# Optimization experiments

Hardware: AMD Instinct MI355X
Metric: run time of the kernel (lower is better)

The kernel has to match this reference:

```python
import jax, jax.numpy as jnp
import numpy as np

N = 30000
E = 480000
F_IN = 16
HID = 64
HEADS = 2
D = HID // HEADS
L = 2
NEG_SLOPE = 0.2


def _edge_softmax(alpha, dst, num_nodes):
    # alpha: [E, HEADS]; softmax over edges sharing the same destination node
    amax = jax.ops.segment_max(alpha, dst, num_segments=num_nodes)
    ex = jnp.exp(alpha - amax[dst])
    den = jax.ops.segment_sum(ex, dst, num_segments=num_nodes)
    return ex / (den[dst] + 1e-16)


def _han_edge(x_src, x_dst, ei, a_src, a_dst, n_dst):
    # x_src: [N_src, HEADS, D], x_dst: [N_dst, HEADS, D], ei: [2, E]
    src, dst = ei[0], ei[1]
    a_s = jnp.einsum('nhd,hd->nh', x_src, a_src)
    a_d = jnp.einsum('nhd,hd->nh', x_dst, a_dst)
    alpha = jax.nn.leaky_relu(a_s[src] + a_d[dst], NEG_SLOPE)  # [E, HEADS]
    alpha = _edge_softmax(alpha, dst, n_dst)
    msg = x_src[src] * alpha[..., None]                        # [E, HEADS, D]
    out = jax.ops.segment_sum(msg, dst, num_segments=n_dst)
    return jax.nn.relu(out.reshape(n_dst, HID))


def _group(xs, q, kw, kb):
    # semantic (cross-relation) attention; xs: list of [N, HID]
    out = jnp.stack(xs)                           # [T, N, HID]
    k = jnp.tanh(out @ kw + kb).mean(axis=1)      # [T, HID]
    attn = jax.nn.softmax(jnp.einsum('f,tf->t', q, k))
    return jnp.einsum('t,tnf->nf', attn, out)


def setup_inputs() -> dict:
    key = jax.random.key(0)
    ks = jax.random.split(key, 24)
    s = 0.1
    f32 = jnp.float32
    return {
        'x_job': jax.random.normal(ks[0], (N, F_IN), f32),
        'x_machine': jax.random.normal(ks[1], (N, F_IN), f32),
        'edge_index_jm': jax.random.randint(ks[2], (2, E), 0, N),
        'edge_index_mj': jax.random.randint(ks[3], (2, E), 0, N),
        'edge_index_jj': jax.random.randint(ks[4], (2, E), 0, N),
        'enc_w_job': jax.random.normal(ks[5], (F_IN, HID), f32) * s,
        'enc_b_job': jax.random.normal(ks[6], (HID,), f32) * s,
        'enc_w_machine': jax.random.normal(ks[7], (F_IN, HID), f32) * s,
        'enc_b_machine': jax.random.normal(ks[8], (HID,), f32) * s,
        'proj_w': jax.random.normal(ks[9], (L, 2, HID, HID), f32) * s,
        'proj_b': jax.random.normal(ks[10], (L, 2, HID), f32) * s,
        'att_src': jax.random.normal(ks[11], (L, 3, HEADS, D), f32) * s,
        'att_dst': jax.random.normal(ks[12], (L, 3, HEADS, D), f32) * s,
        'klin_w': jax.random.normal(ks[13], (L, HID, HID), f32) * s,
        'klin_b': jax.random.normal(ks[14], (L, HID), f32) * s,
        'q_sem': jax.random.normal(ks[15], (L, HID), f32) * s,
        'lin0_w': jax.random.normal(ks[16], (HID, HID), f32) * s,
        'lin0_b': jax.random.normal(ks[17], (HID,), f32) * s,
        'linout_w': jax.random.normal(ks[18], (HID, 16), f32) * s,
        'linout_b': jax.random.normal(ks[19], (16,), f32) * s,
        'linv_w': jax.random.normal(ks[20], (HID, 1), f32) * s,
        'linv_b': jax.random.normal(ks[21], (1,), f32) * s,
    }


def reference(x_job, x_machine, edge_index_jm, edge_index_mj, edge_index_jj,
              enc_w_job, enc_b_job, enc_w_machine, enc_b_machine,
              proj_w, proj_b, att_src, att_dst, klin_w, klin_b, q_sem,
              lin0_w, lin0_b, linout_w, linout_b, linv_w, linv_b):
    # per-node-type encoder: Linear + relu_
    xj = jax.nn.relu(x_job @ enc_w_job + enc_b_job)          # [N, HID]
    xm = jax.nn.relu(x_machine @ enc_w_machine + enc_b_machine)
    for l in range(L):
        pj = (xj @ proj_w[l, 0] + proj_b[l, 0]).reshape(N, HEADS, D)
        pm = (xm @ proj_w[l, 1] + proj_b[l, 1]).reshape(N, HEADS, D)
        # edge-type order follows edge_index_dict iteration: jm, mj, jj
        out_jm = _han_edge(pj, pm, edge_index_jm, att_src[l, 0], att_dst[l, 0], N)
        out_mj = _han_edge(pm, pj, edge_index_mj, att_src[l, 1], att_dst[l, 1], N)
        out_jj = _han_edge(pj, pj, edge_index_jj, att_src[l, 2], att_dst[l, 2], N)
        xj = _group([out_mj, out_jj], q_sem[l], klin_w[l], klin_b[l])
        xm = _group([out_jm], q_sem[l], klin_w[l], klin_b[l])
    full_x = jnp.concatenate([xj, xm], axis=0)               # [2N, HID]
    value = (full_x @ linv_w + linv_b).mean()
    h = full_x @ lin0_w + lin0_b
    action = jnp.tanh(h @ linout_w + linout_b)               # [2N, 16]
    return action, value
```

## Files before the change

### kernel.cpp

```cpp
#include <hip/hip_runtime.h>
#include <math.h>


#define GEMM_GRID 512
#define KRED_GRID 256
#define BUCKET_SHIFT 6
#define BUCKET_NODES 64
#define BUCKET_CAP 1536
#define BIN_CHUNK 2048

__device__ __forceinline__ float4 ld4(const float* __restrict__ p, int idx4)
{
    return ((const float4*)p)[idx4];
}

__device__ __forceinline__ float halfred(float v)
{
#pragma unroll
    for (int off = 16; off; off >>= 1) v += __shfl_xor(v, off);
    return v;
}

struct ProjSide {
    const float* x0; const float* x1; const float* attn;
    const float* W; const float* b; float* p;
    const float* a0v; float* o0; const float* a1v; float* o1;
    const float* a2v; float* o2; const float* a3v; float* o3;
};

__global__ __launch_bounds__(256, 4) void proj2_kernel(ProjSide sa, ProjSide sb, int n)
{
    const ProjSide S = blockIdx.y ? sb : sa;
    __shared__ __align__(16) float xs[16][64];
    int tid = threadIdx.x, lane = tid & 63, wid = tid >> 6;
    float Wreg[64];
#pragma unroll
    for (int k = 0; k < 64; k++) Wreg[k] = S.W[k * 64 + lane];
    float bc = S.b[lane];
    float a0c = S.o0 ? S.a0v[lane] : 0.f;
    float a1c = S.o1 ? S.a1v[lane] : 0.f;
    float a2c = S.o2 ? S.a2v[lane] : 0.f;
    float a3c = S.o3 ? S.a3v[lane] : 0.f;
    float ca0 = 0.f, ca1 = 0.f;
    if (S.x1) { ca0 = S.attn[0]; ca1 = S.attn[1]; }
    int qn = tid >> 4, qq = tid & 15;
    for (int base = blockIdx.x * 16; base < n; base += gridDim.x * 16) {
        __syncthreads();
        int node = base + qn;
        if (node < n) {
            float4 xq;
            if (S.x1) {
                float4 u = ld4(S.x0, node * 16 + qq), v = ld4(S.x1, node * 16 + qq);
                xq.x = ca0 * u.x + ca1 * v.x; xq.y = ca0 * u.y + ca1 * v.y;
                xq.z = ca0 * u.z + ca1 * v.z; xq.w = ca0 * u.w + ca1 * v.w;
            } else {
                xq = ld4(S.x0, node * 16 + qq);
            }
            *(float4*)&xs[qn][qq * 4] = xq;
        }
        __syncthreads();
#pragma unroll
        for (int nd = 0; nd < 4; nd++) {
            int nc = base + wid * 4 + nd;
            if (nc >= n) break;
            float acc = bc;
#pragma unroll
            for (int k4 = 0; k4 < 16; k4++) {
                float4 xv = *(const float4*)&xs[wid * 4 + nd][k4 * 4];
                acc = fmaf(xv.x, Wreg[4 * k4 + 0], acc);
                acc = fmaf(xv.y, Wreg[4 * k4 + 1], acc);
                acc = fmaf(xv.z, Wreg[4 * k4 + 2], acc);
                acc = fmaf(xv.w, Wreg[4 * k4 + 3], acc);
            }
            S.p[nc * 64 + lane] = acc;
            int h = lane >> 5;
            if (S.o0) { float v = halfred(acc * a0c); if ((lane & 31) == 0) S.o0[nc * 2 + h] = v; }
            if (S.o1) { float v = halfred(acc * a1c); if ((lane & 31) == 0) S.o1[nc * 2 + h] = v; }
            if (S.o2) { float v = halfred(acc * a2c); if ((lane & 31) == 0) S.o2[nc * 2 + h] = v; }
            if (S.o3) { float v = halfred(acc * a3c); if ((lane & 31) == 0) S.o3[nc * 2 + h] = v; }
        }
    }
}

struct EncSide {
    const float* x; const float* We; const float* be;
    const float* W; const float* b; float* p;
    const float* a0v; float* o0; const float* a1v; float* o1;
    const float* a2v; float* o2; const float* a3v; float* o3;
};

__global__ __launch_bounds__(256, 4) void encproj2_kernel(EncSide sa, EncSide sb, int n)
{
    const EncSide S = blockIdx.y ? sb : sa;
    __shared__ __align__(16) float xs[16][16];
    __shared__ __align__(16) float es[16][64];
    int tid = threadIdx.x, lane = tid & 63, wid = tid >> 6;
    float Ereg[16];
#pragma unroll
    for (int k = 0; k < 16; k++) Ereg[k] = S.We[k * 64 + lane];
    float Wreg[64];
#pragma unroll
    for (int k = 0; k < 64; k++) Wreg[k] = S.W[k * 64 + lane];
    float ebc = S.be[lane], bc = S.b[lane];
    float a0c = S.o0 ? S.a0v[lane] : 0.f;
    float a1c = S.o1 ? S.a1v[lane] : 0.f;
    float a2c = S.o2 ? S.a2v[lane] : 0.f;
    float a3c = S.o3 ? S.a3v[lane] : 0.f;
    for (int base = blockIdx.x * 16; base < n; base += gridDim.x * 16) {
        __syncthreads();
        if (tid < 64) {
            int nn = tid >> 2, q = tid & 3;
            int node = base + nn;
            if (node < n) *(float4*)&xs[nn][q * 4] = ld4(S.x, node * 4 + q);
        }
        __syncthreads();
#pragma unroll
        for (int nd = 0; nd < 4; nd++) {
            int nc = base + wid * 4 + nd;
            if (nc >= n) break;
            float a = ebc;
#pragma unroll
            for (int k4 = 0; k4 < 4; k4++) {
                float4 xv = *(const float4*)&xs[wid * 4 + nd][k4 * 4];
                a = fmaf(xv.x, Ereg[4 * k4 + 0], a);
                a = fmaf(xv.y, Ereg[4 * k4 + 1], a);
                a = fmaf(xv.z, Ereg[4 * k4 + 2], a);
                a = fmaf(xv.w, Ereg[4 * k4 + 3], a);
            }
            es[wid * 4 + nd][lane] = fmaxf(a, 0.f);
        }
        __syncthreads();
#pragma unroll
        for (int nd = 0; nd < 4; nd++) {
            int nc = base + wid * 4 + nd;
            if (nc >= n) break;
            float acc = bc;
#pragma unroll
            for (int k4 = 0; k4 < 16; k4++) {
                float4 xv = *(const float4*)&es[wid * 4 + nd][k4 * 4];
                acc = fmaf(xv.x, Wreg[4 * k4 + 0], acc);
                acc = fmaf(xv.y, Wreg[4 * k4 + 1], acc);
                acc = fmaf(xv.z, Wreg[4 * k4 + 2], acc);
                acc = fmaf(xv.w, Wreg[4 * k4 + 3], acc);
            }
            S.p[nc * 64 + lane] = acc;
            int h = lane >> 5;
            if (S.o0) { float v = halfred(acc * a0c); if ((lane & 31) == 0) S.o0[nc * 2 + h] = v; }
            if (S.o1) { float v = halfred(acc * a1c); if ((lane & 31) == 0) S.o1[nc * 2 + h] = v; }
            if (S.o2) { float v = halfred(acc * a2c); if ((lane & 31) == 0) S.o2[nc * 2 + h] = v; }
            if (S.o3) { float v = halfred(acc * a3c); if ((lane & 31) == 0) S.o3[nc * 2 + h] = v; }
        }
    }
}

__global__ __launch_bounds__(256) void bin_kernel(
    const int* __restrict__ s0, const int* __restrict__ s1, const int* __restrict__ s2,
    const int* __restrict__ d0, const int* __restrict__ d1, const int* __restrict__ d2,
    int* __restrict__ cursor, int* __restrict__ binned, int e, int nb)
{
    int ty = blockIdx.y;
    const int* s = ty == 0 ? s0 : (ty == 1 ? s1 : s2);
    const int* d = ty == 0 ? d0 : (ty == 1 ? d1 : d2);
    __shared__ int cnt[512], rbase[512];
    int tid = threadIdx.x;
    for (int i = tid; i < nb; i += 256) cnt[i] = 0;
    __syncthreads();
    int beg = blockIdx.x * BIN_CHUNK;
    int end = beg + BIN_CHUNK; if (end > e) end = e;
    for (int i = beg + tid; i < end; i += 256)
        atomicAdd(&cnt[d[i] >> BUCKET_SHIFT], 1);
    __syncthreads();
    for (int i = tid; i < nb; i += 256) {
        rbase[i] = atomicAdd(&cursor[ty * nb + i], cnt[i]);
        cnt[i] = 0;
    }
    __syncthreads();
    int* bb = binned + (size_t)ty * nb * BUCKET_CAP;
    for (int i = beg + tid; i < end; i += 256) {
        int dv = d[i], b = dv >> BUCKET_SHIFT;
        int slot = rbase[b] + atomicAdd(&cnt[b], 1);
        if (slot < BUCKET_CAP)
            bb[b * BUCKET_CAP + slot] = (s[i] << BUCKET_SHIFT) | (dv & (BUCKET_NODES - 1));
    }
}

__global__ void bucketscan_kernel(const int* __restrict__ cursor,
                                  int* __restrict__ bbase, int nb)
{
    int ty = blockIdx.x;
    const int* c = cursor + (size_t)ty * nb;
    int* o = bbase + (size_t)ty * nb;
    int lane = threadIdx.x;
    int carry = 0;
    for (int base = 0; base < nb; base += 64) {
        int i = base + lane;
        int v = (i < nb) ? c[i] : 0;
        int incl = v;
#pragma unroll
        for (int off = 1; off < 64; off <<= 1) {
            int u = __shfl_up(incl, off);
            if (lane >= off) incl += u;
        }
        if (i < nb) o[i] = carry + incl - v;
        carry += __shfl(incl, 63);
    }
}

__global__ __launch_bounds__(256) void bucket_kernel(
    const int* __restrict__ cursor, const int* __restrict__ bbase,
    const int* __restrict__ binned,
    int* __restrict__ rowptr, int* __restrict__ rowend, int* __restrict__ colsrc,
    int n, int nb, int e)
{
    int ty = blockIdx.y, b = blockIdx.x;
    __shared__ int stage[BUCKET_CAP];
    __shared__ int ncnt[64], nexcl[64], ncur[64];
    int tid = threadIdx.x;
    int cnt = cursor[ty * nb + b]; if (cnt > BUCKET_CAP) cnt = BUCKET_CAP;
    int base = bbase[ty * nb + b];
    const int* bb = binned + ((size_t)ty * nb + b) * BUCKET_CAP;
    if (tid < 64) ncnt[tid] = 0;
    __syncthreads();
    for (int i = tid; i < cnt; i += 256) {
        int v = bb[i];
        stage[i] = v;
        atomicAdd(&ncnt[v & (BUCKET_NODES - 1)], 1);
    }
    __syncthreads();
    if (tid < 64) {
        int v = ncnt[tid];
        int incl = v;
#pragma unroll
        for (int off = 1; off < 64; off <<= 1) {
            int u = __shfl_up(incl, off);
            if (tid >= off) incl += u;
        }
        int excl = incl - v;
        nexcl[tid] = excl;
        ncur[tid] = 0;
        int node = (b << BUCKET_SHIFT) + tid;
        if (node < n) {
            rowptr[(size_t)ty * n + node] = base + excl;
            rowend[(size_t)ty * n + node] = base + excl + v;
        }
    }
    __syncthreads();
    int* cs = colsrc + (size_t)ty * e;
    for (int i = tid; i < cnt; i += 256) {
        int v = stage[i];
        int dl = v & (BUCKET_NODES - 1);
        int pos = nexcl[dl] + atomicAdd(&ncur[dl], 1);
        cs[base + pos] = v >> BUCKET_SHIFT;
    }
}

struct AggSide {
    const int* rp; const int* re; const int* cs;
    const float* xsrc; const float* as; const float* ad;
    float* out;
};

__global__ __launch_bounds__(256, 8) void agg3_kernel(AggSide A0, AggSide A1, AggSide A2, int n)
{
    const AggSide A = blockIdx.y == 0 ? A0 : (blockIdx.y == 1 ? A1 : A2);
    __shared__ int ebuf[4][96];
    int tid = threadIdx.x;
    int lane = tid & 63, wid = tid >> 6;
    int node = blockIdx.x * 4 + wid;
    if (node >= n) return;
    int l32 = lane & 31;
    int hh = lane >> 5;
    int g = lane >> 4;
    int q = lane & 15;
    int hq = q >> 3;
    int beg = A.rp[node], end = A.re[node];
    float ad = A.ad[node * 2 + hh];
    float den = 0.f;
    float4 acc = {0.f, 0.f, 0.f, 0.f};
    int* eb = ebuf[wid];
    for (int c = beg; c < end; c += 32) {
        int cnt = end - c; if (cnt > 32) cnt = 32;
        int sl = A.cs[c + (l32 < cnt ? l32 : 0)];
        float w = 0.f;
        if (l32 < cnt) {
            float a = A.as[sl * 2 + hh] + ad;
            a = (a > 0.f) ? a : 0.2f * a;
            w = __expf(a);
        }
        den += w;
        if (lane < 32) eb[l32 * 3] = sl;
        eb[l32 * 3 + 1 + hh] = __float_as_int(w);
        int iters = (cnt + 3) >> 2;
        int it = 0;
        for (; it + 2 <= iters; it += 2) {
            int e0 = it * 4 + g, e1 = e0 + 4;
            int sa = eb[e0 * 3];
            float wa = __int_as_float(eb[e0 * 3 + 1 + hq]);
            int sb = eb[e1 * 3];
            float wb = __int_as_float(eb[e1 * 3 + 1 + hq]);
            float4 xa = ld4(A.xsrc, sa * 16 + q);
            float4 xb = ld4(A.xsrc, sb * 16 + q);
            acc.x = fmaf(wa, xa.x, acc.x);
            acc.y = fmaf(wa, xa.y, acc.y);
            acc.z = fmaf(wa, xa.z, acc.z);
            acc.w = fmaf(wa, xa.w, acc.w);
            acc.x = fmaf(wb, xb.x, acc.x);
            acc.y = fmaf(wb, xb.y, acc.y);
            acc.z = fmaf(wb, xb.z, acc.z);
            acc.w = fmaf(wb, xb.w, acc.w);
        }
        if (it < iters) {
            int e0 = it * 4 + g;
            int sa = eb[e0 * 3];
            float wa = __int_as_float(eb[e0 * 3 + 1 + hq]);
            float4 xa = ld4(A.xsrc, sa * 16 + q);
            acc.x = fmaf(wa, xa.x, acc.x);
            acc.y = fmaf(wa, xa.y, acc.y);
            acc.z = fmaf(wa, xa.z, acc.z);
            acc.w = fmaf(wa, xa.w, acc.w);
        }
    }
    acc.x += __shfl_xor(acc.x, 16);
    acc.y += __shfl_xor(acc.y, 16);
    acc.z += __shfl_xor(acc.z, 16);
    acc.w += __shfl_xor(acc.w, 16);
    acc.x += __shfl_xor(acc.x, 32);
    acc.y += __shfl_xor(acc.y, 32);
    acc.z += __shfl_xor(acc.z, 32);
    acc.w += __shfl_xor(acc.w, 32);
    float dtot = halfred(den);
    float dq = __shfl(dtot, (q >= 8) ? 32 : 0);
    if (g == 0) {
        float r = 1.f / (dq + 1e-16f);
        float4 o;
        o.x = fmaxf(acc.x * r, 0.f);
        o.y = fmaxf(acc.y * r, 0.f);
        o.z = fmaxf(acc.z * r, 0.f);
        o.w = fmaxf(acc.w * r, 0.f);
        *(float4*)&A.out[node * 64 + q * 4] = o;
    }
}

__global__ __launch_bounds__(256, 4) void kred2_kernel(
    const float* __restrict__ xin0, const float* __restrict__ xin1,
    const float* __restrict__ kw, const float* __restrict__ kb,
    float* __restrict__ kacc0, float* __restrict__ kacc1, int n)
{
    const float* xin = blockIdx.y ? xin1 : xin0;
    float* kacc = blockIdx.y ? kacc1 : kacc0;
    __shared__ __align__(16) float xs[16][64];
    __shared__ float red[256];
    int tid = threadIdx.x, lane = tid & 63, wid = tid >> 6;
    float Wreg[64];
#pragma unroll
    for (int k = 0; k < 64; k++) Wreg[k] = kw[k * 64 + lane];
    float bc = kb[lane];
    int qn = tid >> 4, qq = tid & 15;
    float kl = 0.f;
    for (int base = blockIdx.x * 16; base < n; base += gridDim.x * 16) {
        __syncthreads();
        int node = base + qn;
        if (node < n) *(float4*)&xs[qn][qq * 4] = ld4(xin, node * 16 + qq);
        __syncthreads();
#pragma unroll
        for (int nd = 0; nd < 4; nd++) {
            int nc = base + wid * 4 + nd;
            if (nc >= n) break;
            float acc = bc;
#pragma unroll
            for (int k4 = 0; k4 < 16; k4++) {
                float4 xv = *(const float4*)&xs[wid * 4 + nd][k4 * 4];
                acc = fmaf(xv.x, Wreg[4 * k4 + 0], acc);
                acc = fmaf(xv.y, Wreg[4 * k4 + 1], acc);
                acc = fmaf(xv.z, Wreg[4 * k4 + 2], acc);
                acc = fmaf(xv.w, Wreg[4 * k4 + 3], acc);
            }
            kl += tanhf(acc);
        }
    }
    red[tid] = kl;
    __syncthreads();
    if (wid == 0) {
        float s = red[lane] + red[64 + lane] + red[128 + lane] + red[192 + lane];
        atomicAdd(&kacc[lane], s);
    }
}

__global__ void attnfin_kernel(const float* __restrict__ kacc, const float* __restrict__ q,
                               float* __restrict__ attn, float inv_n)
{
    int lane = threadIdx.x;
    float qc = q[lane];
    float v0 = qc * kacc[lane] * inv_n;
    float v1 = qc * kacc[64 + lane] * inv_n;
#pragma unroll
    for (int off = 32; off; off >>= 1) {
        v0 += __shfl_xor(v0, off);
        v1 += __shfl_xor(v1, off);
    }
    if (lane == 0) {
        float m = fmaxf(v0, v1);
        float e0 = expf(v0 - m), e1 = expf(v1 - m);
        float inv = 1.f / (e0 + e1);
        attn[0] = e0 * inv;
        attn[1] = e1 * inv;
    }
}

__global__ __launch_bounds__(256, 4) void final_kernel(
    const float* __restrict__ t0, const float* __restrict__ t1,
    const float* __restrict__ attn, const float* __restrict__ xm,
    const float* __restrict__ w0, const float* __restrict__ b0,
    const float* __restrict__ w1, const float* __restrict__ b1,
    const float* __restrict__ wv,
    float* __restrict__ action, float* __restrict__ vsum, int n)
{
    __shared__ __align__(16) float xs[16][64];
    __shared__ __align__(16) float hs[4][4][68];
    __shared__ float W1s[1024];
    __shared__ float red[256];
    int tid = threadIdx.x, lane = tid & 63, wid = tid >> 6;
    int qn = tid >> 4, qq = tid & 15;
    float W0reg[64];
#pragma unroll
    for (int k = 0; k < 64; k++) W0reg[k] = w0[k * 64 + lane];
    float b0c = b0[lane], b1c = b1[lane & 15];
    float ca0 = attn[0], ca1 = attn[1];
    float4 wvq = ld4(wv, qq);
    for (int i = tid; i < 1024; i += 256) W1s[i] = w1[i];
    float vloc = 0.f;
    int n2 = 2 * n;
    for (int base = blockIdx.x * 16; base < n2; base += gridDim.x * 16) {
        __syncthreads();
        int node = base + qn;
        if (node < n2) {
            float4 xq;
            if (node < n) {
                float4 u = ld4(t0, node * 16 + qq), v = ld4(t1, node * 16 + qq);
                xq.x = ca0 * u.x + ca1 * v.x; xq.y = ca0 * u.y + ca1 * v.y;
                xq.z = ca0 * u.z + ca1 * v.z; xq.w = ca0 * u.w + ca1 * v.w;
            } else {
                xq = ld4(xm, (node - n) * 16 + qq);
            }
            *(float4*)&xs[qn][qq * 4] = xq;
            vloc += xq.x * wvq.x + xq.y * wvq.y + xq.z * wvq.z + xq.w * wvq.w;
        }
        __syncthreads();
#pragma unroll
        for (int nd = 0; nd < 4; nd++) {
            int nc = base + wid * 4 + nd;
            if (nc >= n2) break;
            float acc = b0c;
#pragma unroll
            for (int k4 = 0; k4 < 16; k4++) {
                float4 xv = *(const float4*)&xs[wid * 4 + nd][k4 * 4];
                acc = fmaf(xv.x, W0reg[4 * k4 + 0], acc);
                acc = fmaf(xv.y, W0reg[4 * k4 + 1], acc);
                acc = fmaf(xv.z, W0reg[4 * k4 + 2], acc);
                acc = fmaf(xv.w, W0reg[4 * k4 + 3], acc);
            }
            hs[wid][nd][lane] = acc;
        }
        __syncthreads();
        int nd2 = lane >> 4, c2 = lane & 15;
        int nc2 = base + wid * 4 + nd2;
        if (nc2 < n2) {
            float acc2 = b1c;
#pragma unroll
            for (int k4 = 0; k4 < 16; k4++) {
                float4 hv = *(const float4*)&hs[wid][nd2][k4 * 4];
                acc2 = fmaf(hv.x, W1s[(4 * k4 + 0) * 16 + c2], acc2);
                acc2 = fmaf(hv.y, W1s[(4 * k4 + 1) * 16 + c2], acc2);
                acc2 = fmaf(hv.z, W1s[(4 * k4 + 2) * 16 + c2], acc2);
                acc2 = fmaf(hv.w, W1s[(4 * k4 + 3) * 16 + c2], acc2);
            }
            action[(size_t)nc2 * 16 + c2] = tanhf(acc2);
        }
    }
    red[tid] = vloc;
    __syncthreads();
    for (int s = 128; s; s >>= 1) {
        if (tid < s) red[tid] += red[tid + s];
        __syncthreads();
    }
    if (tid == 0) atomicAdd(vsum, red[0]);
}

__global__ void value_finish_kernel(const float* __restrict__ vsum,
                                    const float* __restrict__ vb,
                                    float* __restrict__ out, int twoN)
{
    if (threadIdx.x == 0 && blockIdx.x == 0)
        out[0] = vsum[0] / (float)twoN + vb[0];
}

extern "C" void kernel_launch(void* const* d_in, const int* in_sizes, int n_in,
                              void* d_out, int out_size, void* d_ws, size_t ws_size,
                              hipStream_t stream)
{
    const int N = in_sizes[0] / 16;
    const int E = in_sizes[2] / 2;
    const int NB = (N + BUCKET_NODES - 1) / BUCKET_NODES;

    auto f = [&](int i) { return (const float*)d_in[i]; };
    const float* x_job = f(0);
    const float* x_mac = f(1);
    const int* ei_jm = (const int*)d_in[2];
    const int* ei_mj = (const int*)d_in[3];
    const int* ei_jj = (const int*)d_in[4];
    const float* enc_wj = f(5);
    const float* enc_bj = f(6);
    const float* enc_wm = f(7);
    const float* enc_bm = f(8);
    const float* proj_w = f(9);
    const float* proj_b = f(10);
    const float* att_src = f(11);
    const float* att_dst = f(12);
    const float* klin_w = f(13);
    const float* klin_b = f(14);
    const float* q_sem = f(15);
    const float* lin0_w = f(16);
    const float* lin0_b = f(17);
    const float* lout_w = f(18);
    const float* lout_b = f(19);
    const float* linv_w = f(20);
    const float* linv_b = f(21);

    float* action = (float*)d_out;
    float* value_out = action + (size_t)2 * N * 16;

    char* base = (char*)d_ws;
    size_t off = 0;
    auto alloc = [&](size_t bytes) -> void* {
        void* p = base + off;
        off += (bytes + 255) & ~(size_t)255;
        return p;
    };
    int* cursor3 = (int*)alloc((size_t)3 * NB * 4);
    float* kacc = (float*)alloc(256 * 4);
    float* vsum = (float*)alloc(4);
    size_t zero_bytes = off;

    int* bbase3 = (int*)alloc((size_t)3 * NB * 4);
    int* rowptr3 = (int*)alloc((size_t)3 * N * 4);
    int* rowend3 = (int*)alloc((size_t)3 * N * 4);
    int* colsrc3 = (int*)alloc((size_t)3 * E * 4);
    float* pj = (float*)alloc((size_t)N * 64 * 4);
    float* pm = (float*)alloc((size_t)N * 64 * 4);
    float* out_jm0 = (float*)alloc((size_t)N * 64 * 4);
    float* out_jm1 = (float*)alloc((size_t)N * 64 * 4);
    float* out_mj = (float*)alloc((size_t)N * 64 * 4);
    float* out_jj = (float*)alloc((size_t)N * 64 * 4);
    float* as_jm = (float*)alloc((size_t)N * 2 * 4);
    float* ad_jm = (float*)alloc((size_t)N * 2 * 4);
    float* as_mj = (float*)alloc((size_t)N * 2 * 4);
    float* ad_mj = (float*)alloc((size_t)N * 2 * 4);
    float* as_jj = (float*)alloc((size_t)N * 2 * 4);
    float* ad_jj = (float*)alloc((size_t)N * 2 * 4);
    float* attn0 = (float*)alloc(2 * 4);
    float* attn1 = (float*)alloc(2 * 4);

    int* binned3 = (int*)pj;

    hipMemsetAsync(d_ws, 0, zero_bytes, stream);

    dim3 blk(256);

    int nchunks = (E + BIN_CHUNK - 1) / BIN_CHUNK;
    bin_kernel<<<dim3(nchunks, 3), blk, 0, stream>>>(
        ei_jm, ei_mj, ei_jj, ei_jm + E, ei_mj + E, ei_jj + E,
        cursor3, binned3, E, NB);
    bucketscan_kernel<<<3, 64, 0, stream>>>(cursor3, bbase3, NB);
    bucket_kernel<<<dim3(NB, 3), blk, 0, stream>>>(
        cursor3, bbase3, binned3, rowptr3, rowend3, colsrc3, N, NB, E);

    const int* rp0 = rowptr3;
    const int* rp1 = rowptr3 + N;
    const int* rp2 = rowptr3 + 2 * N;
    const int* re0 = rowend3;
    const int* re1 = rowend3 + N;
    const int* re2 = rowend3 + 2 * N;
    const int* cs0 = colsrc3;
    const int* cs1 = colsrc3 + E;
    const int* cs2 = colsrc3 + 2 * E;

    int ab = (N + 3) / 4;
    float* out_jm_l[2] = {out_jm0, out_jm1};

    for (int l = 0; l < 2; l++) {
        const float* pwj = proj_w + (size_t)(l * 2 + 0) * 4096;
        const float* pwm = proj_w + (size_t)(l * 2 + 1) * 4096;
        const float* pbj = proj_b + (l * 2 + 0) * 64;
        const float* pbm = proj_b + (l * 2 + 1) * 64;
        const float* as0 = att_src + (l * 3 + 0) * 64;
        const float* as1 = att_src + (l * 3 + 1) * 64;
        const float* as2 = att_src + (l * 3 + 2) * 64;
        const float* ad0 = att_dst + (l * 3 + 0) * 64;
        const float* ad1 = att_dst + (l * 3 + 1) * 64;
        const float* ad2 = att_dst + (l * 3 + 2) * 64;

        if (l == 0) {
            EncSide ja = {x_job, enc_wj, enc_bj, pwj, pbj, pj,
                          as0, as_jm, ad1, ad_mj, as2, as_jj, ad2, ad_jj};
            EncSide ma = {x_mac, enc_wm, enc_bm, pwm, pbm, pm,
                          ad0, ad_jm, as1, as_mj, nullptr, nullptr, nullptr, nullptr};
            encproj2_kernel<<<dim3(GEMM_GRID, 2), blk, 0, stream>>>(ja, ma, N);
        } else {
            ProjSide ja = {out_mj, out_jj, attn0, pwj, pbj, pj,
                           as0, as_jm, ad1, ad_mj, as2, as_jj, ad2, ad_jj};
            ProjSide ma = {out_jm0, nullptr, nullptr, pwm, pbm, pm,
                           ad0, ad_jm, as1, as_mj, nullptr, nullptr, nullptr, nullptr};
            proj2_kernel<<<dim3(GEMM_GRID, 2), blk, 0, stream>>>(ja, ma, N);
        }

        AggSide A0 = {rp0, re0, cs0, pj, as_jm, ad_jm, out_jm_l[l]};
        AggSide A1 = {rp1, re1, cs1, pm, as_mj, ad_mj, out_mj};
        AggSide A2 = {rp2, re2, cs2, pj, as_jj, ad_jj, out_jj};
        agg3_kernel<<<dim3(ab, 3), blk, 0, stream>>>(A0, A1, A2, N);

        const float* kw = klin_w + (size_t)l * 4096;
        const float* kb = klin_b + l * 64;
        float* k0 = kacc + l * 128;
        float* k1 = k0 + 64;
        kred2_kernel<<<dim3(KRED_GRID, 2), blk, 0, stream>>>(out_mj, out_jj, kw, kb, k0, k1, N);
        attnfin_kernel<<<1, 64, 0, stream>>>(k0, q_sem + l * 64, l ? attn1 : attn0,
                                             1.f / (float)N);
    }

    final_kernel<<<GEMM_GRID * 2, blk, 0, stream>>>(out_mj, out_jj, attn1, out_jm1,
                                                    lin0_w, lin0_b, lout_w, lout_b, linv_w,
                                                    action, vsum, N);
    value_finish_kernel<<<1, 64, 0, stream>>>(vsum, linv_b, value_out, 2 * N);
}
```

Baseline: 357.3 us.

## Fold semantic-attention softmax into consumers, widen agg unroll, double GEMM grid

Removes the single-block attnfin kernel launches and has every block of proj2 and final_kernel recompute the two-way semantic softmax from the accumulated key sums. The aggregation kernel moves to separate shared arrays for source indices and per-head weights, and its gather loop is unrolled to four edges per step so more independent loads are in flight. GEMM_GRID is doubled, which also doubles the final_kernel grid. Each block repeats a small reduction, and the larger grid adds per-block weight-load overhead.

```diff
diff --git a/kernel.cpp b/kernel.cpp
--- a/kernel.cpp
+++ b/kernel.cpp
@@ -2,7 +2,7 @@
 #include <math.h>
 
 
-#define GEMM_GRID 512
+#define GEMM_GRID 1024
 #define KRED_GRID 256
 #define BUCKET_SHIFT 6
 #define BUCKET_NODES 64
@@ -21,8 +21,27 @@
     return v;
 }
 
+__device__ __forceinline__ float2 sem_attn(const float* __restrict__ kacc,
+                                           const float* __restrict__ qsem,
+                                           float inv_n, int lane)
+{
+    float qc = qsem[lane];
+    float v0 = qc * kacc[lane] * inv_n;
+    float v1 = qc * kacc[64 + lane] * inv_n;
+#pragma unroll
+    for (int off = 32; off; off >>= 1) {
+        v0 += __shfl_xor(v0, off);
+        v1 += __shfl_xor(v1, off);
+    }
+    float m = fmaxf(v0, v1);
+    float e0 = __expf(v0 - m), e1 = __expf(v1 - m);
+    float inv = 1.f / (e0 + e1);
+    return {e0 * inv, e1 * inv};
+}
+
 struct ProjSide {
-    const float* x0; const float* x1; const float* attn;
+    const float* x0; const float* x1;
+    const float* kacc; const float* qsem; float inv_n;
     const float* W; const float* b; float* p;
     const float* a0v; float* o0; const float* a1v; float* o1;
     const float* a2v; float* o2; const float* a3v; float* o3;
@@ -42,7 +61,10 @@
     float a2c = S.o2 ? S.a2v[lane] : 0.f;
     float a3c = S.o3 ? S.a3v[lane] : 0.f;
     float ca0 = 0.f, ca1 = 0.f;
-    if (S.x1) { ca0 = S.attn[0]; ca1 = S.attn[1]; }
+    if (S.x1) {
+        float2 at = sem_attn(S.kacc, S.qsem, S.inv_n, lane);
+        ca0 = at.x; ca1 = at.y;
+    }
     int qn = tid >> 4, qq = tid & 15;
     for (int base = blockIdx.x * 16; base < n; base += gridDim.x * 16) {
         __syncthreads();
@@ -263,7 +285,8 @@
 __global__ __launch_bounds__(256, 8) void agg3_kernel(AggSide A0, AggSide A1, AggSide A2, int n)
 {
     const AggSide A = blockIdx.y == 0 ? A0 : (blockIdx.y == 1 ? A1 : A2);
-    __shared__ int ebuf[4][96];
+    __shared__ int ebs[4][32];
+    __shared__ float ebw[4][2][32];
     int tid = threadIdx.x;
     int lane = tid & 63, wid = tid >> 6;
     int node = blockIdx.x * 4 + wid;
@@ -277,7 +300,8 @@
     float ad = A.ad[node * 2 + hh];
     float den = 0.f;
     float4 acc = {0.f, 0.f, 0.f, 0.f};
-    int* eb = ebuf[wid];
+    int* es = ebs[wid];
+    float* ew = ebw[wid][0];
     for (int c = beg; c < end; c += 32) {
         int cnt = end - c; if (cnt > 32) cnt = 32;
         int sl = A.cs[c + (l32 < cnt ? l32 : 0)];
@@ -288,36 +312,35 @@
             w = __expf(a);
         }
         den += w;
-        if (lane < 32) eb[l32 * 3] = sl;
-        eb[l32 * 3 + 1 + hh] = __float_as_int(w);
+        if (lane < 32) es[l32] = sl;
+        ew[hh * 32 + l32] = w;
         int iters = (cnt + 3) >> 2;
         int it = 0;
-        for (; it + 2 <= iters; it += 2) {
-            int e0 = it * 4 + g, e1 = e0 + 4;
-            int sa = eb[e0 * 3];
-            float wa = __int_as_float(eb[e0 * 3 + 1 + hq]);
-            int sb = eb[e1 * 3];
-            float wb = __int_as_float(eb[e1 * 3 + 1 + hq]);
-            float4 xa = ld4(A.xsrc, sa * 16 + q);
-            float4 xb = ld4(A.xsrc, sb * 16 + q);
-            acc.x = fmaf(wa, xa.x, acc.x);
-            acc.y = fmaf(wa, xa.y, acc.y);
-            acc.z = fmaf(wa, xa.z, acc.z);
-            acc.w = fmaf(wa, xa.w, acc.w);
-            acc.x = fmaf(wb, xb.x, acc.x);
-            acc.y = fmaf(wb, xb.y, acc.y);
-            acc.z = fmaf(wb, xb.z, acc.z);
-            acc.w = fmaf(wb, xb.w, acc.w);
-        }
-        if (it < iters) {
+        for (; it + 4 <= iters; it += 4) {
             int e0 = it * 4 + g;
-            int sa = eb[e0 * 3];
-            float wa = __int_as_float(eb[e0 * 3 + 1 + hq]);
-            float4 xa = ld4(A.xsrc, sa * 16 + q);
-            acc.x = fmaf(wa, xa.x, acc.x);
-            acc.y = fmaf(wa, xa.y, acc.y);
-            acc.z = fmaf(wa, xa.z, acc.z);
-            acc.w = fmaf(wa, xa.w, acc.w);
+            int s0 = es[e0], s1 = es[e0 + 4], s2 = es[e0 + 8], s3 = es[e0 + 12];
+            float w0 = ew[hq * 32 + e0],     w1 = ew[hq * 32 + e0 + 4];
+            float w2 = ew[hq * 32 + e0 + 8], w3 = ew[hq * 32 + e0 + 12];
+            float4 x0 = ld4(A.xsrc, s0 * 16 + q);
+            float4 x1 = ld4(A.xsrc, s1 * 16 + q);
+            float4 x2 = ld4(A.xsrc, s2 * 16 + q);
+            float4 x3 = ld4(A.xsrc, s3 * 16 + q);
+            acc.x = fmaf(w0, x0.x, acc.x); acc.y = fmaf(w0, x0.y, acc.y);
+            acc.z = fmaf(w0, x0.z, acc.z); acc.w = fmaf(w0, x0.w, acc.w);
+            acc.x = fmaf(w1, x1.x, acc.x); acc.y = fmaf(w1, x1.y, acc.y);
+            acc.z = fmaf(w1, x1.z, acc.z); acc.w = fmaf(w1, x1.w, acc.w);
+            acc.x = fmaf(w2, x2.x, acc.x); acc.y = fmaf(w2, x2.y, acc.y);
+            acc.z = fmaf(w2, x2.z, acc.z); acc.w = fmaf(w2, x2.w, acc.w);
+            acc.x = fmaf(w3, x3.x, acc.x); acc.y = fmaf(w3, x3.y, acc.y);
+            acc.z = fmaf(w3, x3.z, acc.z); acc.w = fmaf(w3, x3.w, acc.w);
+        }
+        for (; it < iters; it++) {
+            int e0 = it * 4 + g;
+            int s0 = es[e0];
+            float w0 = ew[hq * 32 + e0];
+            float4 x0 = ld4(A.xsrc, s0 * 16 + q);
+            acc.x = fmaf(w0, x0.x, acc.x); acc.y = fmaf(w0, x0.y, acc.y);
+            acc.z = fmaf(w0, x0.z, acc.z); acc.w = fmaf(w0, x0.w, acc.w);
         }
     }
     acc.x += __shfl_xor(acc.x, 16);
@@ -386,30 +409,10 @@
     }
 }
 
-__global__ void attnfin_kernel(const float* __restrict__ kacc, const float* __restrict__ q,
-                               float* __restrict__ attn, float inv_n)
-{
-    int lane = threadIdx.x;
-    float qc = q[lane];
-    float v0 = qc * kacc[lane] * inv_n;
-    float v1 = qc * kacc[64 + lane] * inv_n;
-#pragma unroll
-    for (int off = 32; off; off >>= 1) {
-        v0 += __shfl_xor(v0, off);
-        v1 += __shfl_xor(v1, off);
-    }
-    if (lane == 0) {
-        float m = fmaxf(v0, v1);
-        float e0 = expf(v0 - m), e1 = expf(v1 - m);
-        float inv = 1.f / (e0 + e1);
-        attn[0] = e0 * inv;
-        attn[1] = e1 * inv;
-    }
-}
-
 __global__ __launch_bounds__(256, 4) void final_kernel(
     const float* __restrict__ t0, const float* __restrict__ t1,
-    const float* __restrict__ attn, const float* __restrict__ xm,
+    const float* __restrict__ kacc, const float* __restrict__ qsem, float inv_n,
+    const float* __restrict__ xm,
     const float* __restrict__ w0, const float* __restrict__ b0,
     const float* __restrict__ w1, const float* __restrict__ b1,
     const float* __restrict__ wv,
@@ -425,7 +428,8 @@
 #pragma unroll
     for (int k = 0; k < 64; k++) W0reg[k] = w0[k * 64 + lane];
     float b0c = b0[lane], b1c = b1[lane & 15];
-    float ca0 = attn[0], ca1 = attn[1];
+    float2 at = sem_attn(kacc, qsem, inv_n, lane);
+    float ca0 = at.x, ca1 = at.y;
     float4 wvq = ld4(wv, qq);
     for (int i = tid; i < 1024; i += 256) W1s[i] = w1[i];
     float vloc = 0.f;
@@ -557,8 +561,6 @@
     float* ad_mj = (float*)alloc((size_t)N * 2 * 4);
     float* as_jj = (float*)alloc((size_t)N * 2 * 4);
     float* ad_jj = (float*)alloc((size_t)N * 2 * 4);
-    float* attn0 = (float*)alloc(2 * 4);
-    float* attn1 = (float*)alloc(2 * 4);
 
     int* binned3 = (int*)pj;
 
@@ -586,6 +588,7 @@
 
     int ab = (N + 3) / 4;
     float* out_jm_l[2] = {out_jm0, out_jm1};
+    float inv_n = 1.f / (float)N;
 
     for (int l = 0; l < 2; l++) {
         const float* pwj = proj_w + (size_t)(l * 2 + 0) * 4096;
@@ -606,9 +609,9 @@
                           ad0, ad_jm, as1, as_mj, nullptr, nullptr, nullptr, nullptr};
             encproj2_kernel<<<dim3(GEMM_GRID, 2), blk, 0, stream>>>(ja, ma, N);
         } else {
-            ProjSide ja = {out_mj, out_jj, attn0, pwj, pbj, pj,
+            ProjSide ja = {out_mj, out_jj, kacc, q_sem, inv_n, pwj, pbj, pj,
                            as0, as_jm, ad1, ad_mj, as2, as_jj, ad2, ad_jj};
-            ProjSide ma = {out_jm0, nullptr, nullptr, pwm, pbm, pm,
+            ProjSide ma = {out_jm0, nullptr, nullptr, nullptr, 0.f, pwm, pbm, pm,
                            ad0, ad_jm, as1, as_mj, nullptr, nullptr, nullptr, nullptr};
             proj2_kernel<<<dim3(GEMM_GRID, 2), blk, 0, stream>>>(ja, ma, N);
         }
@@ -623,11 +626,11 @@
         float* k0 = kacc + l * 128;
         float* k1 = k0 + 64;
         kred2_kernel<<<dim3(KRED_GRID, 2), blk, 0, stream>>>(out_mj, out_jj, kw, kb, k0, k1, N);
-        attnfin_kernel<<<1, 64, 0, stream>>>(k0, q_sem + l * 64, l ? attn1 : attn0,
-                                             1.f / (float)N);
-    }
-
-    final_kernel<<<GEMM_GRID * 2, blk, 0, stream>>>(out_mj, out_jj, attn1, out_jm1,
+    }
+
+    final_kernel<<<GEMM_GRID * 2, blk, 0, stream>>>(out_mj, out_jj,
+                                                    kacc + 128, q_sem + 64, inv_n,
+                                                    out_jm1,
                                                     lin0_w, lin0_b, lout_w, lout_b, linv_w,
                                                     action, vsum, N);
     value_finish_kernel<<<1, 64, 0, stream>>>(vsum, linv_b, value_out, 2 * N);
```

Result: no change. 361.0 us (+1.0%).
